# Kernel optimization log

Measured on AMD Instinct MI355X. Metric: run time of the kernel, lower is better.

The kernel has to match this reference:

```python
import jax, jax.numpy as jnp
import numpy as np

N = 262144
MUL0, MUL1, MUL2 = 128, 64, 32          # multiplicities of 0e, 1o, 2e
D0, D1, D2 = MUL0, MUL1 * 3, MUL2 * 5   # flat dims: 128, 192, 160
NG = MUL1 + MUL2                        # 96 gate scalars (0e)
NS = MUL0 + NG                          # 224 scalar outputs of the Linear


def _norm2mom_cst(f):
    # e3nn normalize2mom: rescale activation so E_{x~N(0,1)}[f(x)^2] = 1
    xs = np.random.default_rng(0).standard_normal(1_000_000).astype(np.float32)
    return float(1.0 / np.sqrt(np.mean(np.asarray(f(jnp.asarray(xs))) ** 2)))

CST_SILU = _norm2mom_cst(jax.nn.silu)
CST_RELU = _norm2mom_cst(jax.nn.relu)


def setup_inputs() -> dict:
    key = jax.random.key(0)
    k = jax.random.split(key, 5)
    return {
        "x": jax.random.normal(k[0], (N, D0 + D1 + D2), jnp.float32),
        "W0": jax.random.normal(k[1], (MUL0, NS), jnp.float32),
        "b0": jax.random.normal(k[2], (NS,), jnp.float32),
        "W1": jax.random.normal(k[3], (MUL1, MUL1), jnp.float32),
        "W2": jax.random.normal(k[4], (MUL2, MUL2), jnp.float32),
    }


def reference(x, W0, b0, W1, W2):
    n = x.shape[0]
    # split input into irrep blocks: [n,128] 0e, [n,64,3] 1o, [n,32,5] 2e
    x0 = x[:, :D0]
    x1 = x[:, D0:D0 + D1].reshape(n, MUL1, 3)
    x2 = x[:, D0 + D1:].reshape(n, MUL2, 5)
    # e3nn o3.Linear: per-irrep block matmul with 1/sqrt(fan_in) path norm;
    # bias only on scalar (0e) outputs
    s = x0 @ W0 * (1.0 / np.sqrt(MUL0)) + b0                      # [n,224]
    v = jnp.einsum('nim,ij->njm', x1, W1) * (1.0 / np.sqrt(MUL1))  # [n,64,3]
    t = jnp.einsum('nim,ij->njm', x2, W2) * (1.0 / np.sqrt(MUL2))  # [n,32,5]
    # e3nn Gate: silu on the 128 true scalars, relu on the 96 gates,
    # gated irreps multiplied channelwise by their gate scalar
    scalars = CST_SILU * jax.nn.silu(s[:, :MUL0])                  # [n,128]
    gates = CST_RELU * jax.nn.relu(s[:, MUL0:])                    # [n,96]
    gv = (v * gates[:, :MUL1, None]).reshape(n, D1)                # [n,192]
    gt = (t * gates[:, MUL1:, None]).reshape(n, D2)                # [n,160]
    return jnp.concatenate([scalars, gv, gt], axis=-1)            # [n,480]
```

## Files before the change

### kernel.cpp

```cpp
#include <hip/hip_runtime.h>

#define NROWS   262144
#define DIN     480
#define DOUT    480
#define LDW0    224

#define M_TILE  32
#define XSTR    488

#define CST_SILU 1.6765290f
#define CST_RELU 1.4142135623730951f
#define INV_S128 0.08838834764831845f
#define INV_S64  0.125f
#define INV_S32  0.17677669529663687f

#define WS_FRAGS 66
#define WS_BYTES (WS_FRAGS * 64 * 16)

typedef short  bf16x8 __attribute__((ext_vector_type(8)));
typedef short  s16x4  __attribute__((ext_vector_type(4)));
typedef float  f32x4  __attribute__((ext_vector_type(4)));

__device__ __forceinline__ ushort f2bf(float f) {
    unsigned u = __float_as_uint(f);
    u = (u + 0x7FFFu + ((u >> 16) & 1u)) >> 16;
    return (ushort)u;
}
__device__ __forceinline__ float bf2f(ushort h) {
    return __uint_as_float(((unsigned)h) << 16);
}

__device__ __forceinline__ bf16x8 load_b_frag(const float* __restrict__ W, int ldw,
                                              int kbase, int nbase, int lane) {
    int n  = nbase + (lane & 15);
    int k0 = kbase + ((lane >> 4) << 3);
    bf16x8 f;
#pragma unroll
    for (int e = 0; e < 8; ++e) f[e] = (short)f2bf(W[(k0 + e) * ldw + n]);
    return f;
}

__global__ __launch_bounds__(64) void prep_frags(
        const float* __restrict__ W0, const float* __restrict__ W1,
        const float* __restrict__ W2, ushort* __restrict__ ws) {
    const int b = blockIdx.x, lane = threadIdx.x;
    const int lr = lane & 15, kg = lane >> 4;
    const float* W; int ldw, n, k0;
    if (b < 56)      { W = W0; ldw = 224; n = (b >> 2) * 16 + lr; k0 = (b & 3) * 32 + (kg << 3); }
    else if (b < 64) { int t = b - 56; W = W1; ldw = 64; n = (t >> 1) * 16 + lr; k0 = (t & 1) * 32 + (kg << 3); }
    else             { W = W2; ldw = 32; n = (b - 64) * 16 + lr; k0 = (kg << 3); }
    bf16x8 f;
#pragma unroll
    for (int e = 0; e < 8; ++e) f[e] = (short)f2bf(W[(k0 + e) * ldw + n]);
    *reinterpret_cast<bf16x8*>(ws + (b * 64 + lane) * 8) = f;
}

template <bool PRE>
__global__ __launch_bounds__(256, 5) void percep_kernel(
        const float* __restrict__ x,  const float* __restrict__ W0,
        const float* __restrict__ b0, const float* __restrict__ W1,
        const float* __restrict__ W2, float* __restrict__ out,
        const ushort* __restrict__ ws) {
    __shared__ __align__(16) ushort xs[M_TILE * XSTR];

    const int tid  = threadIdx.x;
    const int lane = tid & 63;
    const int wid  = tid >> 6;
    const int lr   = lane & 15;
    const int kg   = lane >> 4;
    const int row0 = blockIdx.x * M_TILE;
    const bf16x8* F = reinterpret_cast<const bf16x8*>(ws);

#pragma unroll
    for (int it = 0; it < 4; ++it) {
        int idx = tid + it * 256;
        int row = idx >> 5, c4 = idx & 31;
        const float4 v = reinterpret_cast<const float4*>(x + (row0 + row) * DIN)[c4];
        s16x4 o = { (short)f2bf(v.x), (short)f2bf(v.y), (short)f2bf(v.z), (short)f2bf(v.w) };
        *reinterpret_cast<s16x4*>(&xs[row * XSTR + c4 * 4]) = o;
    }
#pragma unroll
    for (int it = 0; it < 2; ++it) {
        int idx = tid + it * 256;
        int row = idx >> 4, g = idx & 15;
        const float4* p = reinterpret_cast<const float4*>(x + (row0 + row) * DIN + 128 + 12 * g);
        float4 q0 = p[0], q1 = p[1], q2 = p[2];
        float v[12] = { q0.x, q0.y, q0.z, q0.w, q1.x, q1.y, q1.z, q1.w, q2.x, q2.y, q2.z, q2.w };
#pragma unroll
        for (int m = 0; m < 3; ++m) {
            s16x4 o = { (short)f2bf(v[m]), (short)f2bf(v[m + 3]),
                        (short)f2bf(v[m + 6]), (short)f2bf(v[m + 9]) };
            *reinterpret_cast<s16x4*>(&xs[row * XSTR + 128 + 64 * m + 4 * g]) = o;
        }
    }
    {
        int row = tid >> 3, g = tid & 7;
        const float4* p = reinterpret_cast<const float4*>(x + (row0 + row) * DIN + 320 + 20 * g);
        float4 q0 = p[0], q1 = p[1], q2 = p[2], q3 = p[3], q4 = p[4];
        float v[20] = { q0.x, q0.y, q0.z, q0.w, q1.x, q1.y, q1.z, q1.w, q2.x, q2.y, q2.z, q2.w,
                        q3.x, q3.y, q3.z, q3.w, q4.x, q4.y, q4.z, q4.w };
#pragma unroll
        for (int m = 0; m < 5; ++m) {
            s16x4 o = { (short)f2bf(v[m]), (short)f2bf(v[m + 5]),
                        (short)f2bf(v[m + 10]), (short)f2bf(v[m + 15]) };
            *reinterpret_cast<s16x4*>(&xs[row * XSTR + 320 + 32 * m + 4 * g]) = o;
        }
    }
    __syncthreads();

    bf16x8 aS[2][4];
#pragma unroll
    for (int rf = 0; rf < 2; ++rf)
#pragma unroll
        for (int kk = 0; kk < 4; ++kk)
            aS[rf][kk] = *reinterpret_cast<const bf16x8*>(
                &xs[(rf * 16 + lr) * XSTR + kk * 32 + (kg << 3)]);
    __syncthreads();

    int sbase, scount, vu, tu;
    if      (wid == 0) { sbase = 0;  scount = 4; vu = 0; tu = -1; }
    else if (wid == 1) { sbase = 4;  scount = 4; vu = 1; tu = -1; }
    else if (wid == 2) { sbase = 8;  scount = 3; vu = 2; tu = 0;  }
    else               { sbase = 11; scount = 3; vu = 3; tu = 1;  }

    for (int t = 0; t < scount; ++t) {
        int st  = sbase + t;
        int col = st * 16 + lr;
        bf16x8 bS[4];
#pragma unroll
        for (int kk = 0; kk < 4; ++kk)
            bS[kk] = PRE ? F[(st * 4 + kk) * 64 + lane]
                         : load_b_frag(W0, LDW0, kk * 32, st * 16, lane);
        float bias = b0[col];
#pragma unroll
        for (int rf = 0; rf < 2; ++rf) {
            f32x4 acc = { 0.f, 0.f, 0.f, 0.f };
#pragma unroll
            for (int kk = 0; kk < 4; ++kk)
                acc = __builtin_amdgcn_mfma_f32_16x16x32_bf16(aS[rf][kk], bS[kk], acc, 0, 0, 0);
            int rbase = rf * 16 + (kg << 2);
            if (st < 8) {
#pragma unroll
                for (int r = 0; r < 4; ++r) {
                    float s = acc[r] * INV_S128 + bias;
                    out[(row0 + rbase + r) * DOUT + col] = CST_SILU * s / (1.f + __expf(-s));
                }
            } else {
#pragma unroll
                for (int r = 0; r < 4; ++r) {
                    float s = acc[r] * INV_S128 + bias;
                    xs[(rbase + r) * XSTR + (col - 128)] = f2bf(CST_RELU * fmaxf(s, 0.f));
                }
            }
        }
    }
    __syncthreads();

    {
        bf16x8 bV[2];
#pragma unroll
        for (int kk = 0; kk < 2; ++kk)
            bV[kk] = PRE ? F[(56 + vu * 2 + kk) * 64 + lane]
                         : load_b_frag(W1, 64, kk * 32, vu * 16, lane);
        int j = vu * 16 + lr;
#pragma unroll
        for (int rf = 0; rf < 2; ++rf) {
            f32x4 acc0 = {0,0,0,0}, acc1 = {0,0,0,0}, acc2 = {0,0,0,0};
#pragma unroll
            for (int kk = 0; kk < 2; ++kk) {
                const ushort* base = &xs[(rf * 16 + lr) * XSTR + 128 + kk * 32 + (kg << 3)];
                acc0 = __builtin_amdgcn_mfma_f32_16x16x32_bf16(
                    *reinterpret_cast<const bf16x8*>(base +   0), bV[kk], acc0, 0, 0, 0);
                acc1 = __builtin_amdgcn_mfma_f32_16x16x32_bf16(
                    *reinterpret_cast<const bf16x8*>(base +  64), bV[kk], acc1, 0, 0, 0);
                acc2 = __builtin_amdgcn_mfma_f32_16x16x32_bf16(
                    *reinterpret_cast<const bf16x8*>(base + 128), bV[kk], acc2, 0, 0, 0);
            }
#pragma unroll
            for (int r = 0; r < 4; ++r) {
                int row = rf * 16 + (kg << 2) + r;
                float g = bf2f(xs[row * XSTR + j]) * INV_S64;
                float* po = out + (row0 + row) * DOUT + 128 + 3 * j;
                po[0] = acc0[r] * g; po[1] = acc1[r] * g; po[2] = acc2[r] * g;
            }
        }
    }

    if (tu >= 0) {
        bf16x8 bT = PRE ? F[(64 + tu) * 64 + lane]
                        : load_b_frag(W2, 32, 0, tu * 16, lane);
        int j = tu * 16 + lr;
#pragma unroll
        for (int rf = 0; rf < 2; ++rf) {
            const ushort* base = &xs[(rf * 16 + lr) * XSTR + 320 + (kg << 3)];
            f32x4 z = {0,0,0,0};
            f32x4 a0 = __builtin_amdgcn_mfma_f32_16x16x32_bf16(*reinterpret_cast<const bf16x8*>(base +   0), bT, z, 0, 0, 0);
            f32x4 a1 = __builtin_amdgcn_mfma_f32_16x16x32_bf16(*reinterpret_cast<const bf16x8*>(base +  32), bT, z, 0, 0, 0);
            f32x4 a2 = __builtin_amdgcn_mfma_f32_16x16x32_bf16(*reinterpret_cast<const bf16x8*>(base +  64), bT, z, 0, 0, 0);
            f32x4 a3 = __builtin_amdgcn_mfma_f32_16x16x32_bf16(*reinterpret_cast<const bf16x8*>(base +  96), bT, z, 0, 0, 0);
            f32x4 a4 = __builtin_amdgcn_mfma_f32_16x16x32_bf16(*reinterpret_cast<const bf16x8*>(base + 128), bT, z, 0, 0, 0);
#pragma unroll
            for (int r = 0; r < 4; ++r) {
                int row = rf * 16 + (kg << 2) + r;
                float g = bf2f(xs[row * XSTR + 64 + j]) * INV_S32;
                float* po = out + (row0 + row) * DOUT + 320 + 5 * j;
                po[0] = a0[r] * g; po[1] = a1[r] * g; po[2] = a2[r] * g;
                po[3] = a3[r] * g; po[4] = a4[r] * g;
            }
        }
    }
}

extern "C" void kernel_launch(void* const* d_in, const int* in_sizes, int n_in,
                              void* d_out, int out_size, void* d_ws, size_t ws_size,
                              hipStream_t stream) {
    const float* x  = (const float*)d_in[0];
    const float* W0 = (const float*)d_in[1];
    const float* b0 = (const float*)d_in[2];
    const float* W1 = (const float*)d_in[3];
    const float* W2 = (const float*)d_in[4];
    float* out = (float*)d_out;
    dim3 grid(NROWS / M_TILE), block(256);
    if (ws_size >= WS_BYTES) {
        hipLaunchKernelGGL(prep_frags, dim3(WS_FRAGS), dim3(64), 0, stream, W0, W1, W2, (ushort*)d_ws);
        hipLaunchKernelGGL((percep_kernel<true>), grid, block, 0, stream,
                           x, W0, b0, W1, W2, out, (const ushort*)d_ws);
    } else {
        hipLaunchKernelGGL((percep_kernel<false>), grid, block, 0, stream,
                           x, W0, b0, W1, W2, out, (const ushort*)d_ws);
    }
}
```

Before: 224.2 us.

## Keep gate scalars in registers and load scalar A fragments directly from global

Scalar-part A fragments are now read straight from global memory into registers instead of being staged through LDS. The shared tile shrinks to hold only the vector and tensor blocks, and occupancy is raised to 6 blocks. Gate tiles are remapped so each wave computes the gate columns it later needs and keeps them in registers, which removes one barrier and the bf16 round-trip of gates through LDS. The cost is extra register pressure and less evenly balanced work across waves.

Result: slower. 274.1 us (+22.2%).

```diff
diff --git a/kernel.cpp b/kernel.cpp
--- a/kernel.cpp
+++ b/kernel.cpp
@@ -3,10 +3,9 @@
 #define NROWS   262144
 #define DIN     480
 #define DOUT    480
-#define LDW0    224
 
 #define M_TILE  32
-#define XSTR    488
+#define XSTR    360
 
 #define CST_SILU 1.6765290f
 #define CST_RELU 1.4142135623730951f
@@ -17,17 +16,14 @@
 #define WS_FRAGS 66
 #define WS_BYTES (WS_FRAGS * 64 * 16)
 
-typedef short  bf16x8 __attribute__((ext_vector_type(8)));
-typedef short  s16x4  __attribute__((ext_vector_type(4)));
-typedef float  f32x4  __attribute__((ext_vector_type(4)));
+typedef short bf16x8 __attribute__((ext_vector_type(8)));
+typedef short s16x4  __attribute__((ext_vector_type(4)));
+typedef float f32x4  __attribute__((ext_vector_type(4)));
 
 __device__ __forceinline__ ushort f2bf(float f) {
     unsigned u = __float_as_uint(f);
     u = (u + 0x7FFFu + ((u >> 16) & 1u)) >> 16;
     return (ushort)u;
-}
-__device__ __forceinline__ float bf2f(ushort h) {
-    return __uint_as_float(((unsigned)h) << 16);
 }
 
 __device__ __forceinline__ bf16x8 load_b_frag(const float* __restrict__ W, int ldw,
@@ -56,9 +52,9 @@
 }
 
 template <bool PRE>
-__global__ __launch_bounds__(256, 5) void percep_kernel(
+__global__ __launch_bounds__(256, 6) void percep_kernel(
         const float* __restrict__ x,  const float* __restrict__ W0,
-        const float* __restrict__ b0, const float* __restrict__ W1,
+        const float* __restrict__ bias0, const float* __restrict__ W1,
         const float* __restrict__ W2, float* __restrict__ out,
         const ushort* __restrict__ ws) {
     __shared__ __align__(16) ushort xs[M_TILE * XSTR];
@@ -72,14 +68,6 @@
     const bf16x8* F = reinterpret_cast<const bf16x8*>(ws);
 
 #pragma unroll
-    for (int it = 0; it < 4; ++it) {
-        int idx = tid + it * 256;
-        int row = idx >> 5, c4 = idx & 31;
-        const float4 v = reinterpret_cast<const float4*>(x + (row0 + row) * DIN)[c4];
-        s16x4 o = { (short)f2bf(v.x), (short)f2bf(v.y), (short)f2bf(v.z), (short)f2bf(v.w) };
-        *reinterpret_cast<s16x4*>(&xs[row * XSTR + c4 * 4]) = o;
-    }
-#pragma unroll
     for (int it = 0; it < 2; ++it) {
         int idx = tid + it * 256;
         int row = idx >> 4, g = idx & 15;
@@ -90,7 +78,7 @@
         for (int m = 0; m < 3; ++m) {
             s16x4 o = { (short)f2bf(v[m]), (short)f2bf(v[m + 3]),
                         (short)f2bf(v[m + 6]), (short)f2bf(v[m + 9]) };
-            *reinterpret_cast<s16x4*>(&xs[row * XSTR + 128 + 64 * m + 4 * g]) = o;
+            *reinterpret_cast<s16x4*>(&xs[row * XSTR + 64 * m + 4 * g]) = o;
         }
     }
     {
@@ -103,106 +91,115 @@
         for (int m = 0; m < 5; ++m) {
             s16x4 o = { (short)f2bf(v[m]), (short)f2bf(v[m + 5]),
                         (short)f2bf(v[m + 10]), (short)f2bf(v[m + 15]) };
-            *reinterpret_cast<s16x4*>(&xs[row * XSTR + 320 + 32 * m + 4 * g]) = o;
-        }
-    }
+            *reinterpret_cast<s16x4*>(&xs[row * XSTR + 192 + 32 * m + 4 * g]) = o;
+        }
+    }
+
+    bf16x8 aS[2][4];
+#pragma unroll
+    for (int rf = 0; rf < 2; ++rf)
+#pragma unroll
+        for (int kk = 0; kk < 4; ++kk) {
+            const float4* p = reinterpret_cast<const float4*>(
+                x + (row0 + rf * 16 + lr) * DIN + kk * 32 + (kg << 3));
+            float4 u0 = p[0], u1 = p[1];
+            bf16x8 a = { (short)f2bf(u0.x), (short)f2bf(u0.y), (short)f2bf(u0.z), (short)f2bf(u0.w),
+                         (short)f2bf(u1.x), (short)f2bf(u1.y), (short)f2bf(u1.z), (short)f2bf(u1.w) };
+            aS[rf][kk] = a;
+        }
+
+    f32x4 gV[2], gT[2];
+
+    auto gate_tile = [&](int st, f32x4* g) {
+        bf16x8 b[4];
+#pragma unroll
+        for (int kk = 0; kk < 4; ++kk)
+            b[kk] = PRE ? F[(st * 4 + kk) * 64 + lane]
+                        : load_b_frag(W0, 224, kk * 32, st * 16, lane);
+        float bias = bias0[st * 16 + lr];
+#pragma unroll
+        for (int rf = 0; rf < 2; ++rf) {
+            f32x4 acc = { 0.f, 0.f, 0.f, 0.f };
+#pragma unroll
+            for (int kk = 0; kk < 4; ++kk)
+                acc = __builtin_amdgcn_mfma_f32_16x16x32_bf16(aS[rf][kk], b[kk], acc, 0, 0, 0);
+#pragma unroll
+            for (int r = 0; r < 4; ++r) {
+                float s = acc[r] * INV_S128 + bias;
+                g[rf][r] = fmaxf(s, 0.f) * CST_RELU;
+            }
+        }
+    };
+    auto silu_tile = [&](int st) {
+        bf16x8 b[4];
+#pragma unroll
+        for (int kk = 0; kk < 4; ++kk)
+            b[kk] = PRE ? F[(st * 4 + kk) * 64 + lane]
+                        : load_b_frag(W0, 224, kk * 32, st * 16, lane);
+        float bias = bias0[st * 16 + lr];
+#pragma unroll
+        for (int rf = 0; rf < 2; ++rf) {
+            f32x4 acc = { 0.f, 0.f, 0.f, 0.f };
+#pragma unroll
+            for (int kk = 0; kk < 4; ++kk)
+                acc = __builtin_amdgcn_mfma_f32_16x16x32_bf16(aS[rf][kk], b[kk], acc, 0, 0, 0);
+#pragma unroll
+            for (int r = 0; r < 4; ++r) {
+                float s = acc[r] * INV_S128 + bias;
+                float val = CST_SILU * s * __builtin_amdgcn_rcpf(1.f + __expf(-s));
+                out[(row0 + rf * 16 + (kg << 2) + r) * DOUT + st * 16 + lr] = val;
+            }
+        }
+    };
+
+    if      (wid == 0) { gate_tile(8,  gV); gate_tile(12, gT); silu_tile(0); }
+    else if (wid == 1) { gate_tile(9,  gV); gate_tile(13, gT); silu_tile(1); }
+    else if (wid == 2) { gate_tile(10, gV); silu_tile(2); silu_tile(3); silu_tile(4); }
+    else               { gate_tile(11, gV); silu_tile(5); silu_tile(6); silu_tile(7); }
+
     __syncthreads();
 
-    bf16x8 aS[2][4];
-#pragma unroll
-    for (int rf = 0; rf < 2; ++rf)
-#pragma unroll
-        for (int kk = 0; kk < 4; ++kk)
-            aS[rf][kk] = *reinterpret_cast<const bf16x8*>(
-                &xs[(rf * 16 + lr) * XSTR + kk * 32 + (kg << 3)]);
-    __syncthreads();
-
-    int sbase, scount, vu, tu;
-    if      (wid == 0) { sbase = 0;  scount = 4; vu = 0; tu = -1; }
-    else if (wid == 1) { sbase = 4;  scount = 4; vu = 1; tu = -1; }
-    else if (wid == 2) { sbase = 8;  scount = 3; vu = 2; tu = 0;  }
-    else               { sbase = 11; scount = 3; vu = 3; tu = 1;  }
-
-    for (int t = 0; t < scount; ++t) {
-        int st  = sbase + t;
-        int col = st * 16 + lr;
-        bf16x8 bS[4];
-#pragma unroll
-        for (int kk = 0; kk < 4; ++kk)
-            bS[kk] = PRE ? F[(st * 4 + kk) * 64 + lane]
-                         : load_b_frag(W0, LDW0, kk * 32, st * 16, lane);
-        float bias = b0[col];
-#pragma unroll
-        for (int rf = 0; rf < 2; ++rf) {
-            f32x4 acc = { 0.f, 0.f, 0.f, 0.f };
-#pragma unroll
-            for (int kk = 0; kk < 4; ++kk)
-                acc = __builtin_amdgcn_mfma_f32_16x16x32_bf16(aS[rf][kk], bS[kk], acc, 0, 0, 0);
-            int rbase = rf * 16 + (kg << 2);
-            if (st < 8) {
-#pragma unroll
-                for (int r = 0; r < 4; ++r) {
-                    float s = acc[r] * INV_S128 + bias;
-                    out[(row0 + rbase + r) * DOUT + col] = CST_SILU * s / (1.f + __expf(-s));
-                }
-            } else {
-#pragma unroll
-                for (int r = 0; r < 4; ++r) {
-                    float s = acc[r] * INV_S128 + bias;
-                    xs[(rbase + r) * XSTR + (col - 128)] = f2bf(CST_RELU * fmaxf(s, 0.f));
-                }
-            }
-        }
-    }
-    __syncthreads();
-
     {
-        bf16x8 bV[2];
-#pragma unroll
-        for (int kk = 0; kk < 2; ++kk)
-            bV[kk] = PRE ? F[(56 + vu * 2 + kk) * 64 + lane]
-                         : load_b_frag(W1, 64, kk * 32, vu * 16, lane);
-        int j = vu * 16 + lr;
-#pragma unroll
-        for (int rf = 0; rf < 2; ++rf) {
-            f32x4 acc0 = {0,0,0,0}, acc1 = {0,0,0,0}, acc2 = {0,0,0,0};
-#pragma unroll
-            for (int kk = 0; kk < 2; ++kk) {
-                const ushort* base = &xs[(rf * 16 + lr) * XSTR + 128 + kk * 32 + (kg << 3)];
-                acc0 = __builtin_amdgcn_mfma_f32_16x16x32_bf16(
-                    *reinterpret_cast<const bf16x8*>(base +   0), bV[kk], acc0, 0, 0, 0);
-                acc1 = __builtin_amdgcn_mfma_f32_16x16x32_bf16(
-                    *reinterpret_cast<const bf16x8*>(base +  64), bV[kk], acc1, 0, 0, 0);
-                acc2 = __builtin_amdgcn_mfma_f32_16x16x32_bf16(
-                    *reinterpret_cast<const bf16x8*>(base + 128), bV[kk], acc2, 0, 0, 0);
-            }
+        const int vu = wid;
+        bf16x8 bv0 = PRE ? F[(56 + vu * 2) * 64 + lane]     : load_b_frag(W1, 64, 0,  vu * 16, lane);
+        bf16x8 bv1 = PRE ? F[(56 + vu * 2 + 1) * 64 + lane] : load_b_frag(W1, 64, 32, vu * 16, lane);
+        const int j = vu * 16 + lr;
+#pragma unroll
+        for (int rf = 0; rf < 2; ++rf) {
+            const ushort* base = &xs[(rf * 16 + lr) * XSTR + (kg << 3)];
+            f32x4 a0 = {0,0,0,0}, a1 = {0,0,0,0}, a2 = {0,0,0,0};
+            a0 = __builtin_amdgcn_mfma_f32_16x16x32_bf16(*reinterpret_cast<const bf16x8*>(base +   0), bv0, a0, 0, 0, 0);
+            a0 = __builtin_amdgcn_mfma_f32_16x16x32_bf16(*reinterpret_cast<const bf16x8*>(base +  32), bv1, a0, 0, 0, 0);
+            a1 = __builtin_amdgcn_mfma_f32_16x16x32_bf16(*reinterpret_cast<const bf16x8*>(base +  64), bv0, a1, 0, 0, 0);
+            a1 = __builtin_amdgcn_mfma_f32_16x16x32_bf16(*reinterpret_cast<const bf16x8*>(base +  96), bv1, a1, 0, 0, 0);
+            a2 = __builtin_amdgcn_mfma_f32_16x16x32_bf16(*reinterpret_cast<const bf16x8*>(base + 128), bv0, a2, 0, 0, 0);
+            a2 = __builtin_amdgcn_mfma_f32_16x16x32_bf16(*reinterpret_cast<const bf16x8*>(base + 160), bv1, a2, 0, 0, 0);
 #pragma unroll
             for (int r = 0; r < 4; ++r) {
                 int row = rf * 16 + (kg << 2) + r;
-                float g = bf2f(xs[row * XSTR + j]) * INV_S64;
+                float g = gV[rf][r] * INV_S64;
                 float* po = out + (row0 + row) * DOUT + 128 + 3 * j;
-                po[0] = acc0[r] * g; po[1] = acc1[r] * g; po[2] = acc2[r] * g;
-            }
-        }
-    }
-
-    if (tu >= 0) {
-        bf16x8 bT = PRE ? F[(64 + tu) * 64 + lane]
-                        : load_b_frag(W2, 32, 0, tu * 16, lane);
-        int j = tu * 16 + lr;
-#pragma unroll
-        for (int rf = 0; rf < 2; ++rf) {
-            const ushort* base = &xs[(rf * 16 + lr) * XSTR + 320 + (kg << 3)];
+                po[0] = a0[r] * g; po[1] = a1[r] * g; po[2] = a2[r] * g;
+            }
+        }
+    }
+
+    if (wid < 2) {
+        bf16x8 bt = PRE ? F[(64 + wid) * 64 + lane] : load_b_frag(W2, 32, 0, wid * 16, lane);
+        const int j = wid * 16 + lr;
+#pragma unroll
+        for (int rf = 0; rf < 2; ++rf) {
+            const ushort* base = &xs[(rf * 16 + lr) * XSTR + 192 + (kg << 3)];
             f32x4 z = {0,0,0,0};
-            f32x4 a0 = __builtin_amdgcn_mfma_f32_16x16x32_bf16(*reinterpret_cast<const bf16x8*>(base +   0), bT, z, 0, 0, 0);
-            f32x4 a1 = __builtin_amdgcn_mfma_f32_16x16x32_bf16(*reinterpret_cast<const bf16x8*>(base +  32), bT, z, 0, 0, 0);
-            f32x4 a2 = __builtin_amdgcn_mfma_f32_16x16x32_bf16(*reinterpret_cast<const bf16x8*>(base +  64), bT, z, 0, 0, 0);
-            f32x4 a3 = __builtin_amdgcn_mfma_f32_16x16x32_bf16(*reinterpret_cast<const bf16x8*>(base +  96), bT, z, 0, 0, 0);
-            f32x4 a4 = __builtin_amdgcn_mfma_f32_16x16x32_bf16(*reinterpret_cast<const bf16x8*>(base + 128), bT, z, 0, 0, 0);
+            f32x4 a0 = __builtin_amdgcn_mfma_f32_16x16x32_bf16(*reinterpret_cast<const bf16x8*>(base +   0), bt, z, 0, 0, 0);
+            f32x4 a1 = __builtin_amdgcn_mfma_f32_16x16x32_bf16(*reinterpret_cast<const bf16x8*>(base +  32), bt, z, 0, 0, 0);
+            f32x4 a2 = __builtin_amdgcn_mfma_f32_16x16x32_bf16(*reinterpret_cast<const bf16x8*>(base +  64), bt, z, 0, 0, 0);
+            f32x4 a3 = __builtin_amdgcn_mfma_f32_16x16x32_bf16(*reinterpret_cast<const bf16x8*>(base +  96), bt, z, 0, 0, 0);
+            f32x4 a4 = __builtin_amdgcn_mfma_f32_16x16x32_bf16(*reinterpret_cast<const bf16x8*>(base + 128), bt, z, 0, 0, 0);
 #pragma unroll
             for (int r = 0; r < 4; ++r) {
                 int row = rf * 16 + (kg << 2) + r;
-                float g = bf2f(xs[row * XSTR + 64 + j]) * INV_S32;
+                float g = gT[rf][r] * INV_S32;
                 float* po = out + (row0 + row) * DOUT + 320 + 5 * j;
                 po[0] = a0[r] * g; po[1] = a1[r] * g; po[2] = a2[r] * g;
                 po[3] = a3[r] * g; po[4] = a4[r] * g;
```
